# Kernel tuning notes

Measured on AMD Instinct MI355X. Metric: run time of the kernel, lower is better.

Reference implementation:

```python
import jax, jax.numpy as jnp
import numpy as np

NUM_CODES = 1024
CODE_DIM = 256
TEMPERATURE = 1.0  # forward default, clamped to >= 0.01 in original


def setup_inputs() -> dict:
    key = jax.random.key(0)
    k_z, k_e = jax.random.split(key)
    z = jax.random.normal(k_z, (16, 4096, CODE_DIM), dtype=jnp.float32)
    # embed buffer initialized as randn * 0.5 in the torch module
    embed = jax.random.normal(k_e, (NUM_CODES, CODE_DIM), dtype=jnp.float32) * 0.5
    return {"z": z, "embed": embed}


def reference(z, embed):
    K, D = embed.shape
    orig_shape = z.shape
    flat_z = z.reshape(-1, D)                      # [B, D]
    B = flat_z.shape[0]

    dist = (
        jnp.sum(flat_z * flat_z, axis=1, keepdims=True)
        - 2.0 * (flat_z @ embed.T)
        + jnp.sum(embed * embed, axis=1)[None, :]
    )

    soft_assign = jax.nn.softmax(-dist / max(TEMPERATURE, 0.01), axis=-1)  # [B, K]
    codes = jnp.argmin(dist, axis=1)               # [B]
    z_q = embed[codes]                             # [B, D] gather

    sg = jax.lax.stop_gradient
    commitment_loss = jnp.mean((flat_z - sg(z_q)) ** 2)
    codebook_loss = jnp.mean((z_q - sg(flat_z)) ** 2)

    avg_soft = jnp.mean(soft_assign, axis=0)       # [K]
    usage_entropy = -jnp.sum(avg_soft * jnp.log(avg_soft + 1e-10))
    diversity_loss = -usage_entropy / np.log(K).astype(np.float32)

    # straight-through estimator
    z_q_st = (flat_z + sg(z_q - flat_z)).reshape(orig_shape)
    codes_out = codes.reshape(orig_shape[:-1])

    # hard usage / perplexity (scatter-add instead of BxK one-hot)
    counts = jnp.zeros((K,), dtype=jnp.float32).at[codes].add(1.0)
    hard_avg = counts / jnp.asarray(B, dtype=jnp.float32)
    perplexity = jnp.exp(-jnp.sum(hard_avg * jnp.log(hard_avg + 1e-10)))

    return (z_q_st, codes_out, commitment_loss, codebook_loss,
            diversity_loss, usage_entropy, perplexity)
```

## Files before the change

### kernel.cpp

```cpp
#include <hip/hip_runtime.h>
#include <math.h>

typedef _Float16 half8 __attribute__((ext_vector_type(8)));
typedef float f32x4 __attribute__((ext_vector_type(4)));

#define AS1 __attribute__((address_space(1)))
#define AS3 __attribute__((address_space(3)))

#define BTOT   65536
#define DDIM   256
#define KC     1024

__global__ void vq_e2(const float* __restrict__ embed, float* __restrict__ e2g) {
    int gt = blockIdx.x * blockDim.x + threadIdx.x;
    int k = gt >> 6;
    int lane = gt & 63;
    float4 v = *(const float4*)(embed + (size_t)k * DDIM + lane * 4);
    float s = v.x * v.x + v.y * v.y + v.z * v.z + v.w * v.w;
    #pragma unroll
    for (int off = 1; off < 64; off <<= 1) s += __shfl_xor(s, off);
    if (lane == 0) e2g[k] = s;
}

__global__ void vq_prep(const float* __restrict__ embed, char* __restrict__ wsB) {
    int id = blockIdx.x * 256 + threadIdx.x;
    int c  = id >> 5;
    int kc = (id >> 2) & 7;
    int s  = id & 3;
    const float* src = embed + (size_t)c * DDIM + kc * 32 + s * 8;
    half8 hi, lo;
    #pragma unroll
    for (int j = 0; j < 8; ++j) {
        float xv = src[j];
        _Float16 hh = (_Float16)xv;
        hi[j] = hh;
        lo[j] = (_Float16)(xv - (float)hh);
    }
    int q = c >> 8, cl = c & 255;
    int inner = cl * 64 + ((s ^ ((cl >> 1) & 3)) << 4);
    *(half8*)(wsB + (size_t)(kc * 8 + q) * 16384 + inner) = hi;
    *(half8*)(wsB + (size_t)(kc * 8 + 4 + q) * 16384 + inner) = lo;
}

__global__ __launch_bounds__(512, 2)
void vq_main(const float* __restrict__ z, const char* __restrict__ wsB,
             const float* __restrict__ e2g, float* __restrict__ psum_g,
             float* __restrict__ counts_g, float* __restrict__ distsum_g,
             float* __restrict__ codes_f_out)
{
    __shared__ __align__(16) char ldsA[65536];
    __shared__ __align__(16) char ldsBraw[65536];
    float* lmax     = (float*)ldsBraw;
    int*   larg     = (int*)(ldsBraw + 2048);
    float* lsum     = (float*)(ldsBraw + 4096);
    float* rowM     = (float*)(ldsBraw + 6144);
    float* rowInv   = (float*)(ldsBraw + 6400);
    float* psum_lds = (float*)(ldsBraw + 8192);

    const int tid  = threadIdx.x;
    const int w    = tid >> 6;
    const int lane = tid & 63;
    const int row0 = blockIdx.x * 64;
    const int swz   = ((lane >> 4) ^ ((lane >> 1) & 3)) << 4;
    const int aBase = (lane & 15) * 64 + swz;
    const int bBase = w * 2048 + (lane & 15) * 64 + swz;

    #pragma unroll
    for (int ps = 0; ps < 3; ++ps) {
        const char* gs = wsB + (size_t)ps * 16384 + tid * 16;
        char* ld = ldsBraw + ps * 16384 + tid * 16;
        __builtin_amdgcn_global_load_lds((AS1 const void*)gs, (AS3 void*)ld, 16, 0, 0);
        __builtin_amdgcn_global_load_lds((AS1 const void*)(gs + 8192),
                                         (AS3 void*)(ld + 8192), 16, 0, 0);
    }

    {
        const int ar = tid >> 3;
        const int kc = tid & 7;
        const float* src = z + (size_t)(row0 + ar) * DDIM + kc * 32;
        float x[32];
        #pragma unroll
        for (int j = 0; j < 8; ++j) {
            float4 v = ((const float4*)src)[j];
            x[4*j] = v.x; x[4*j+1] = v.y; x[4*j+2] = v.z; x[4*j+3] = v.w;
        }
        float zsq = 0.f;
        #pragma unroll
        for (int j = 0; j < 32; ++j) zsq = fmaf(x[j], x[j], zsq);
        #pragma unroll
        for (int off = 1; off < 64; off <<= 1) zsq += __shfl_xor(zsq, off);
        if (lane == 0) atomicAdd(distsum_g, zsq);
        #pragma unroll
        for (int s = 0; s < 4; ++s) {
            half8 hi, lo;
            #pragma unroll
            for (int j = 0; j < 8; ++j) {
                float xv = x[8*s + j];
                _Float16 hh = (_Float16)xv;
                hi[j] = hh;
                lo[j] = (_Float16)(xv - (float)hh);
            }
            int off = kc * 4096 + ar * 64 + ((s ^ ((ar >> 1) & 3)) << 4);
            *(half8*)(ldsA + off) = hi;
            *(half8*)(ldsA + 32768 + off) = lo;
        }
    }
    __syncthreads();

    f32x4 acc[4][8];
    #pragma unroll
    for (int rt = 0; rt < 4; ++rt)
        #pragma unroll
        for (int cg = 0; cg < 8; ++cg)
            acc[rt][cg] = (f32x4){0.f, 0.f, 0.f, 0.f};

    half8 aHi[4], aLo[4];

    #pragma unroll
    for (int s = 0; s < 64; ++s) {
        const int kc = s >> 3, p = (s >> 2) & 1, q = s & 3;
        if (s < 62)      asm volatile("s_waitcnt vmcnt(4)\n\ts_barrier" ::: "memory");
        else if (s == 62) asm volatile("s_waitcnt vmcnt(2)\n\ts_barrier" ::: "memory");
        else              asm volatile("s_waitcnt vmcnt(0)\n\ts_barrier" ::: "memory");
        if (s + 3 < 64) {
            const char* gs = wsB + (size_t)(s + 3) * 16384 + tid * 16;
            char* ld = ldsBraw + ((s + 3) & 3) * 16384 + tid * 16;
            __builtin_amdgcn_global_load_lds((AS1 const void*)gs, (AS3 void*)ld, 16, 0, 0);
            __builtin_amdgcn_global_load_lds((AS1 const void*)(gs + 8192),
                                             (AS3 void*)(ld + 8192), 16, 0, 0);
        }
        if (p == 0 && q == 0) {
            #pragma unroll
            for (int rt = 0; rt < 4; ++rt) {
                aHi[rt] = *(const half8*)(ldsA + kc * 4096 + rt * 1024 + aBase);
                aLo[rt] = *(const half8*)(ldsA + 32768 + kc * 4096 + rt * 1024 + aBase);
            }
        }
        const char* bb = ldsBraw + (s & 3) * 16384 + bBase;
        #pragma unroll
        for (int ct = 0; ct < 2; ++ct) {
            half8 bf = *(const half8*)(bb + ct * 1024);
            const int cg = q * 2 + ct;
            #pragma unroll
            for (int rt = 0; rt < 4; ++rt) {
                acc[rt][cg] = __builtin_amdgcn_mfma_f32_16x16x32_f16(
                    aHi[rt], bf, acc[rt][cg], 0, 0, 0);
                if (p == 0)
                    acc[rt][cg] = __builtin_amdgcn_mfma_f32_16x16x32_f16(
                        aLo[rt], bf, acc[rt][cg], 0, 0, 0);
            }
        }
    }
    __syncthreads();

    int colv[8];
    float e2v[8];
    #pragma unroll
    for (int cg = 0; cg < 8; ++cg) {
        colv[cg] = (cg >> 1) * 256 + w * 32 + (cg & 1) * 16 + (lane & 15);
        e2v[cg] = e2g[colv[cg]];
    }
    psum_lds[tid] = 0.f;
    psum_lds[tid + 512] = 0.f;
    #pragma unroll
    for (int rt = 0; rt < 4; ++rt) {
        #pragma unroll
        for (int i = 0; i < 4; ++i) {
            float m = -INFINITY; int am = 0x7fffffff;
            #pragma unroll
            for (int cg = 0; cg < 8; ++cg) {
                float l = fmaf(2.f, acc[rt][cg][i], -e2v[cg]);
                if (l > m) { m = l; am = colv[cg]; }
            }
            #pragma unroll
            for (int off = 1; off < 16; off <<= 1) {
                float om = __shfl_xor(m, off);
                int   oa = __shfl_xor(am, off);
                if (om > m || (om == m && oa < am)) { m = om; am = oa; }
            }
            if ((lane & 15) == 0) {
                int r = rt * 16 + ((lane >> 4) << 2) + i;
                lmax[r * 8 + w] = m; larg[r * 8 + w] = am;
            }
        }
    }
    __syncthreads();
    if (tid < 64) {
        float M = -INFINITY; int A = 0x7fffffff;
        #pragma unroll
        for (int ww = 0; ww < 8; ++ww) {
            float mm = lmax[tid * 8 + ww]; int aa = larg[tid * 8 + ww];
            if (mm > M || (mm == M && aa < A)) { M = mm; A = aa; }
        }
        rowM[tid] = M;
        codes_f_out[row0 + tid] = (float)A;
        atomicAdd(&counts_g[A], 1.0f);
        float negm = -M;
        #pragma unroll
        for (int off = 1; off < 64; off <<= 1) negm += __shfl_xor(negm, off);
        if (tid == 0) atomicAdd(distsum_g, negm);
    }
    __syncthreads();
    #pragma unroll
    for (int rt = 0; rt < 4; ++rt) {
        #pragma unroll
        for (int i = 0; i < 4; ++i) {
            const int r = rt * 16 + ((lane >> 4) << 2) + i;
            float M = rowM[r];
            float ss = 0.f;
            #pragma unroll
            for (int cg = 0; cg < 8; ++cg) {
                float e = __expf(fmaf(2.f, acc[rt][cg][i], -e2v[cg]) - M);
                acc[rt][cg][i] = e;
                ss += e;
            }
            #pragma unroll
            for (int off = 1; off < 16; off <<= 1) ss += __shfl_xor(ss, off);
            if ((lane & 15) == 0) lsum[r * 8 + w] = ss;
        }
    }
    __syncthreads();
    if (tid < 64) {
        float S = 0.f;
        #pragma unroll
        for (int ww = 0; ww < 8; ++ww) S += lsum[tid * 8 + ww];
        rowInv[tid] = 1.0f / S;
    }
    __syncthreads();
    #pragma unroll
    for (int cg = 0; cg < 8; ++cg) {
        float cp = 0.f;
        #pragma unroll
        for (int rt = 0; rt < 4; ++rt)
            #pragma unroll
            for (int i = 0; i < 4; ++i)
                cp = fmaf(acc[rt][cg][i], rowInv[rt * 16 + ((lane >> 4) << 2) + i], cp);
        atomicAdd(&psum_lds[colv[cg]], cp);
    }
    __syncthreads();
    atomicAdd(&psum_g[tid], psum_lds[tid]);
    atomicAdd(&psum_g[tid + 512], psum_lds[tid + 512]);
}

__global__ void vq_gather(const float* __restrict__ embed,
                          const float* __restrict__ codes_f,
                          float* __restrict__ outq)
{
    int idx = blockIdx.x * 256 + threadIdx.x;
    int b = idx >> 6;
    int c = (int)codes_f[b];
    ((float4*)outq)[idx] = ((const float4*)embed)[(c << 6) + (idx & 63)];
}

__global__ void vq_finalize(const float* __restrict__ psum_g,
                            const float* __restrict__ counts_g,
                            const float* __restrict__ distsum_g,
                            float* __restrict__ out_s)
{
    __shared__ float s1[16], s2[16];
    int tid = threadIdx.x;
    float a = psum_g[tid] * (1.0f / 65536.0f);
    float e1 = -a * logf(a + 1e-10f);
    float h = counts_g[tid] * (1.0f / 65536.0f);
    float e2 = -h * logf(h + 1e-10f);
    #pragma unroll
    for (int off = 1; off < 64; off <<= 1) {
        e1 += __shfl_xor(e1, off);
        e2 += __shfl_xor(e2, off);
    }
    int w = tid >> 6, lane = tid & 63;
    if (lane == 0) { s1[w] = e1; s2[w] = e2; }
    __syncthreads();
    if (tid == 0) {
        float E1 = 0.0f, E2 = 0.0f;
        #pragma unroll
        for (int i = 0; i < 16; ++i) { E1 += s1[i]; E2 += s2[i]; }
        float commit = distsum_g[0] * (1.0f / 16777216.0f);
        out_s[0] = commit;
        out_s[1] = commit;
        out_s[2] = -E1 / 6.9314718055994531f;
        out_s[3] = E1;
        out_s[4] = __expf(E2);
    }
}

extern "C" void kernel_launch(void* const* d_in, const int* in_sizes, int n_in,
                              void* d_out, int out_size, void* d_ws, size_t ws_size,
                              hipStream_t stream) {
    const float* z     = (const float*)d_in[0];
    const float* embed = (const float*)d_in[1];

    float* out      = (float*)d_out;
    float* zq_out   = out;
    float* codes_f  = out + 16777216;
    float* scalars  = out + 16842752;

    float* ws        = (float*)d_ws;
    float* psum_g    = ws;
    float* counts_g  = ws + 1024;
    float* e2g       = ws + 2048;
    float* distsum_g = ws + 3072;
    char*  wsB       = (char*)d_ws + 16384;

    hipMemsetAsync(d_ws, 0, 3080 * sizeof(float), stream);
    vq_prep<<<128, 256, 0, stream>>>(embed, wsB);
    vq_e2<<<256, 256, 0, stream>>>(embed, e2g);
    vq_main<<<BTOT / 64, 512, 0, stream>>>(z, wsB, e2g, psum_g, counts_g,
                                           distsum_g, codes_f);
    vq_gather<<<4194304 / 256, 256, 0, stream>>>(embed, codes_f, zq_out);
    vq_finalize<<<1, 1024, 0, stream>>>(psum_g, counts_g, distsum_g, scalars);
}
```

Baseline: 224.4 us.

## Read codebook fragments directly from global memory and use 16-wave blocks

Drops the pipelined global-to-LDS staging of the fp16 hi/lo codebook tiles and their per-stage barriers. Each wave now loads its B fragments straight from a re-laid-out workspace into registers. Blocks grow to 1024 threads, so each wave owns 64 codebook columns instead of 128, halving the accumulator registers and allowing more resident waves. The intent is to remove barrier stalls and LDS traffic. The cost is that global/L2 load latency is no longer explicitly prefetched and every block rereads the full codebook from cache.

```diff
diff --git a/kernel.cpp b/kernel.cpp
--- a/kernel.cpp
+++ b/kernel.cpp
@@ -3,9 +3,6 @@
 
 typedef _Float16 half8 __attribute__((ext_vector_type(8)));
 typedef float f32x4 __attribute__((ext_vector_type(4)));
-
-#define AS1 __attribute__((address_space(1)))
-#define AS3 __attribute__((address_space(3)))
 
 #define BTOT   65536
 #define DDIM   256
@@ -36,139 +33,118 @@
         hi[j] = hh;
         lo[j] = (_Float16)(xv - (float)hh);
     }
-    int q = c >> 8, cl = c & 255;
-    int inner = cl * 64 + ((s ^ ((cl >> 1) & 3)) << 4);
-    *(half8*)(wsB + (size_t)(kc * 8 + q) * 16384 + inner) = hi;
-    *(half8*)(wsB + (size_t)(kc * 8 + 4 + q) * 16384 + inner) = lo;
-}
-
-__global__ __launch_bounds__(512, 2)
+    int g = c >> 4;
+    size_t base = ((size_t)((g * 8 + kc) * 2) << 10) + (c & 15) * 16 + s * 256;
+    *(half8*)(wsB + base) = hi;
+    *(half8*)(wsB + base + 1024) = lo;
+}
+
+__global__ __launch_bounds__(1024, 4)
 void vq_main(const float* __restrict__ z, const char* __restrict__ wsB,
              const float* __restrict__ e2g, float* __restrict__ psum_g,
              float* __restrict__ counts_g, float* __restrict__ distsum_g,
              float* __restrict__ codes_f_out)
 {
     __shared__ __align__(16) char ldsA[65536];
-    __shared__ __align__(16) char ldsBraw[65536];
-    float* lmax     = (float*)ldsBraw;
-    int*   larg     = (int*)(ldsBraw + 2048);
-    float* lsum     = (float*)(ldsBraw + 4096);
-    float* rowM     = (float*)(ldsBraw + 6144);
-    float* rowInv   = (float*)(ldsBraw + 6400);
-    float* psum_lds = (float*)(ldsBraw + 8192);
+    float* lmax     = (float*)ldsA;
+    int*   larg     = (int*)(ldsA + 4096);
+    float* lsum     = (float*)(ldsA + 8192);
+    float* rowM     = (float*)(ldsA + 12288);
+    float* rowInv   = (float*)(ldsA + 12544);
+    float* psum_lds = (float*)(ldsA + 16384);
 
     const int tid  = threadIdx.x;
     const int w    = tid >> 6;
     const int lane = tid & 63;
     const int row0 = blockIdx.x * 64;
-    const int swz   = ((lane >> 4) ^ ((lane >> 1) & 3)) << 4;
-    const int aBase = (lane & 15) * 64 + swz;
-    const int bBase = w * 2048 + (lane & 15) * 64 + swz;
-
-    #pragma unroll
-    for (int ps = 0; ps < 3; ++ps) {
-        const char* gs = wsB + (size_t)ps * 16384 + tid * 16;
-        char* ld = ldsBraw + ps * 16384 + tid * 16;
-        __builtin_amdgcn_global_load_lds((AS1 const void*)gs, (AS3 void*)ld, 16, 0, 0);
-        __builtin_amdgcn_global_load_lds((AS1 const void*)(gs + 8192),
-                                         (AS3 void*)(ld + 8192), 16, 0, 0);
-    }
+    const int aBase = (lane & 15) * 64 + (((lane >> 4) ^ ((lane >> 1) & 3)) << 4);
 
     {
-        const int ar = tid >> 3;
-        const int kc = tid & 7;
-        const float* src = z + (size_t)(row0 + ar) * DDIM + kc * 32;
-        float x[32];
-        #pragma unroll
-        for (int j = 0; j < 8; ++j) {
+        const int ar = tid >> 4;
+        const int kp = tid & 15;
+        const float* src = z + (size_t)(row0 + ar) * DDIM + kp * 16;
+        float x[16];
+        #pragma unroll
+        for (int j = 0; j < 4; ++j) {
             float4 v = ((const float4*)src)[j];
             x[4*j] = v.x; x[4*j+1] = v.y; x[4*j+2] = v.z; x[4*j+3] = v.w;
         }
         float zsq = 0.f;
         #pragma unroll
-        for (int j = 0; j < 32; ++j) zsq = fmaf(x[j], x[j], zsq);
+        for (int j = 0; j < 16; ++j) zsq = fmaf(x[j], x[j], zsq);
         #pragma unroll
         for (int off = 1; off < 64; off <<= 1) zsq += __shfl_xor(zsq, off);
         if (lane == 0) atomicAdd(distsum_g, zsq);
-        #pragma unroll
-        for (int s = 0; s < 4; ++s) {
+        const int kc = kp >> 1;
+        #pragma unroll
+        for (int jj = 0; jj < 2; ++jj) {
+            int s = (kp & 1) * 2 + jj;
             half8 hi, lo;
             #pragma unroll
             for (int j = 0; j < 8; ++j) {
-                float xv = x[8*s + j];
+                float xv = x[jj * 8 + j];
                 _Float16 hh = (_Float16)xv;
                 hi[j] = hh;
                 lo[j] = (_Float16)(xv - (float)hh);
             }
-            int off = kc * 4096 + ar * 64 + ((s ^ ((ar >> 1) & 3)) << 4);
+            int off = kc * 8192 + ar * 64 + ((s ^ ((ar >> 1) & 3)) << 4);
             *(half8*)(ldsA + off) = hi;
-            *(half8*)(ldsA + 32768 + off) = lo;
-        }
-    }
-    __syncthreads();
-
-    f32x4 acc[4][8];
+            *(half8*)(ldsA + 4096 + off) = lo;
+        }
+    }
+    __syncthreads();
+
+    f32x4 acc[4][4];
     #pragma unroll
     for (int rt = 0; rt < 4; ++rt)
         #pragma unroll
-        for (int cg = 0; cg < 8; ++cg)
+        for (int cg = 0; cg < 4; ++cg)
             acc[rt][cg] = (f32x4){0.f, 0.f, 0.f, 0.f};
 
-    half8 aHi[4], aLo[4];
-
-    #pragma unroll
-    for (int s = 0; s < 64; ++s) {
-        const int kc = s >> 3, p = (s >> 2) & 1, q = s & 3;
-        if (s < 62)      asm volatile("s_waitcnt vmcnt(4)\n\ts_barrier" ::: "memory");
-        else if (s == 62) asm volatile("s_waitcnt vmcnt(2)\n\ts_barrier" ::: "memory");
-        else              asm volatile("s_waitcnt vmcnt(0)\n\ts_barrier" ::: "memory");
-        if (s + 3 < 64) {
-            const char* gs = wsB + (size_t)(s + 3) * 16384 + tid * 16;
-            char* ld = ldsBraw + ((s + 3) & 3) * 16384 + tid * 16;
-            __builtin_amdgcn_global_load_lds((AS1 const void*)gs, (AS3 void*)ld, 16, 0, 0);
-            __builtin_amdgcn_global_load_lds((AS1 const void*)(gs + 8192),
-                                             (AS3 void*)(ld + 8192), 16, 0, 0);
-        }
-        if (p == 0 && q == 0) {
-            #pragma unroll
-            for (int rt = 0; rt < 4; ++rt) {
-                aHi[rt] = *(const half8*)(ldsA + kc * 4096 + rt * 1024 + aBase);
-                aLo[rt] = *(const half8*)(ldsA + 32768 + kc * 4096 + rt * 1024 + aBase);
-            }
-        }
-        const char* bb = ldsBraw + (s & 3) * 16384 + bBase;
-        #pragma unroll
-        for (int ct = 0; ct < 2; ++ct) {
-            half8 bf = *(const half8*)(bb + ct * 1024);
-            const int cg = q * 2 + ct;
-            #pragma unroll
-            for (int rt = 0; rt < 4; ++rt) {
+    for (int kc = 0; kc < 8; ++kc) {
+        half8 aHi[4], aLo[4];
+        #pragma unroll
+        for (int rt = 0; rt < 4; ++rt) {
+            aHi[rt] = *(const half8*)(ldsA + kc * 8192 + rt * 1024 + aBase);
+            aLo[rt] = *(const half8*)(ldsA + kc * 8192 + 4096 + rt * 1024 + aBase);
+        }
+        #pragma unroll
+        for (int cg = 0; cg < 4; ++cg) {
+            const char* bp = wsB + ((size_t)(((w * 4 + cg) * 8 + kc) * 2) << 10)
+                                 + (lane << 4);
+            half8 bHi = *(const half8*)bp;
+            half8 bLo = *(const half8*)(bp + 1024);
+            #pragma unroll
+            for (int rt = 0; rt < 4; ++rt)
                 acc[rt][cg] = __builtin_amdgcn_mfma_f32_16x16x32_f16(
-                    aHi[rt], bf, acc[rt][cg], 0, 0, 0);
-                if (p == 0)
-                    acc[rt][cg] = __builtin_amdgcn_mfma_f32_16x16x32_f16(
-                        aLo[rt], bf, acc[rt][cg], 0, 0, 0);
-            }
-        }
-    }
-    __syncthreads();
-
-    int colv[8];
-    float e2v[8];
-    #pragma unroll
-    for (int cg = 0; cg < 8; ++cg) {
-        colv[cg] = (cg >> 1) * 256 + w * 32 + (cg & 1) * 16 + (lane & 15);
+                    aHi[rt], bHi, acc[rt][cg], 0, 0, 0);
+            #pragma unroll
+            for (int rt = 0; rt < 4; ++rt)
+                acc[rt][cg] = __builtin_amdgcn_mfma_f32_16x16x32_f16(
+                    aLo[rt], bHi, acc[rt][cg], 0, 0, 0);
+            #pragma unroll
+            for (int rt = 0; rt < 4; ++rt)
+                acc[rt][cg] = __builtin_amdgcn_mfma_f32_16x16x32_f16(
+                    aHi[rt], bLo, acc[rt][cg], 0, 0, 0);
+        }
+    }
+    __syncthreads();
+
+    int colv[4];
+    float e2v[4];
+    #pragma unroll
+    for (int cg = 0; cg < 4; ++cg) {
+        colv[cg] = w * 64 + cg * 16 + (lane & 15);
         e2v[cg] = e2g[colv[cg]];
     }
     psum_lds[tid] = 0.f;
-    psum_lds[tid + 512] = 0.f;
     #pragma unroll
     for (int rt = 0; rt < 4; ++rt) {
         #pragma unroll
         for (int i = 0; i < 4; ++i) {
             float m = -INFINITY; int am = 0x7fffffff;
             #pragma unroll
-            for (int cg = 0; cg < 8; ++cg) {
+            for (int cg = 0; cg < 4; ++cg) {
                 float l = fmaf(2.f, acc[rt][cg][i], -e2v[cg]);
                 if (l > m) { m = l; am = colv[cg]; }
             }
@@ -180,7 +156,7 @@
             }
             if ((lane & 15) == 0) {
                 int r = rt * 16 + ((lane >> 4) << 2) + i;
-                lmax[r * 8 + w] = m; larg[r * 8 + w] = am;
+                lmax[r * 16 + w] = m; larg[r * 16 + w] = am;
             }
         }
     }
@@ -188,8 +164,8 @@
     if (tid < 64) {
         float M = -INFINITY; int A = 0x7fffffff;
         #pragma unroll
-        for (int ww = 0; ww < 8; ++ww) {
-            float mm = lmax[tid * 8 + ww]; int aa = larg[tid * 8 + ww];
+        for (int ww = 0; ww < 16; ++ww) {
+            float mm = lmax[tid * 16 + ww]; int aa = larg[tid * 16 + ww];
             if (mm > M || (mm == M && aa < A)) { M = mm; A = aa; }
         }
         rowM[tid] = M;
@@ -209,26 +185,26 @@
             float M = rowM[r];
             float ss = 0.f;
             #pragma unroll
-            for (int cg = 0; cg < 8; ++cg) {
+            for (int cg = 0; cg < 4; ++cg) {
                 float e = __expf(fmaf(2.f, acc[rt][cg][i], -e2v[cg]) - M);
                 acc[rt][cg][i] = e;
                 ss += e;
             }
             #pragma unroll
             for (int off = 1; off < 16; off <<= 1) ss += __shfl_xor(ss, off);
-            if ((lane & 15) == 0) lsum[r * 8 + w] = ss;
+            if ((lane & 15) == 0) lsum[r * 16 + w] = ss;
         }
     }
     __syncthreads();
     if (tid < 64) {
         float S = 0.f;
         #pragma unroll
-        for (int ww = 0; ww < 8; ++ww) S += lsum[tid * 8 + ww];
+        for (int ww = 0; ww < 16; ++ww) S += lsum[tid * 16 + ww];
         rowInv[tid] = 1.0f / S;
     }
     __syncthreads();
     #pragma unroll
-    for (int cg = 0; cg < 8; ++cg) {
+    for (int cg = 0; cg < 4; ++cg) {
         float cp = 0.f;
         #pragma unroll
         for (int rt = 0; rt < 4; ++rt)
@@ -239,7 +215,6 @@
     }
     __syncthreads();
     atomicAdd(&psum_g[tid], psum_lds[tid]);
-    atomicAdd(&psum_g[tid + 512], psum_lds[tid + 512]);
 }
 
 __global__ void vq_gather(const float* __restrict__ embed,
@@ -305,8 +280,8 @@
     hipMemsetAsync(d_ws, 0, 3080 * sizeof(float), stream);
     vq_prep<<<128, 256, 0, stream>>>(embed, wsB);
     vq_e2<<<256, 256, 0, stream>>>(embed, e2g);
-    vq_main<<<BTOT / 64, 512, 0, stream>>>(z, wsB, e2g, psum_g, counts_g,
-                                           distsum_g, codes_f);
+    vq_main<<<BTOT / 64, 1024, 0, stream>>>(z, wsB, e2g, psum_g, counts_g,
+                                            distsum_g, codes_f);
     vq_gather<<<4194304 / 256, 256, 0, stream>>>(embed, codes_f, zq_out);
     vq_finalize<<<1, 1024, 0, stream>>>(psum_g, counts_g, distsum_g, scalars);
 }
```

Result: slower. 335.5 us (+49.5%).
